# Kernel optimization log

Measured on AMD Instinct MI355X. Metric: run time of the kernel, lower is better.

The kernel has to match this reference:

```python
import jax, jax.numpy as jnp
import numpy as np

B, S, R = 8, 4096, 512
E, K, ATOMS, XAR, TOPK = 64, 256, 16, 3, 2
TEMP = 1.0


def setup_inputs() -> dict:
    key = jax.random.key(0)
    k0, k1, k2, k3, k4 = jax.random.split(key, 5)
    x_latent = jax.random.normal(k0, (B, S, R), jnp.float32)
    router_w = jax.random.normal(k1, (E, R), jnp.float32) * (1.0 / np.sqrt(R))
    atoms = jax.random.normal(k2, (E, ATOMS, R), jnp.float32) * 0.01
    combo_weights = jax.random.uniform(k3, (E, K, XAR), jnp.float32) * 0.5 + 0.25
    combo_logits = jax.random.normal(k4, (E, K, XAR, ATOMS), jnp.float32) * 0.01
    return {"x_latent": x_latent, "router_w": router_w, "atoms": atoms,
            "combo_weights": combo_weights, "combo_logits": combo_logits}


def _expert_centroids(atoms, combo_weights, combo_logits):
    # Hard codeword path (vectorized over experts):
    # sign atoms -> pick argmax atom per (k, xor slot) -> weight -> sum -> sign -> mean over k
    binary = jnp.sign(atoms)                                   # [E, A, R]
    # softmax(logits/t) then argmax == argmax(logits) (monotone)
    idx = jnp.argmax(combo_logits, axis=-1)                    # [E, K, XAR]
    sel = binary[jnp.arange(E)[:, None, None], idx]            # [E, K, XAR, R]
    codewords = jnp.sign((sel * combo_weights[..., None]).sum(axis=2))  # [E, K, R]
    return codewords.mean(axis=1)                              # [E, R]


def reference(x_latent, router_w, atoms, combo_weights, combo_logits):
    t = max(TEMP, 0.1)
    router_logits = jnp.einsum('bsr,er->bse', x_latent, router_w)   # [B, S, E]
    probs_t = jax.nn.softmax(router_logits / t, axis=-1)
    gates, expert_ids = jax.lax.top_k(probs_t, TOPK)                # [B, S, 2]
    gates = gates / gates.sum(axis=-1, keepdims=True)

    centroids = _expert_centroids(atoms, combo_weights, combo_logits)  # [E, R]

    # aux load-balancing loss (uses untempered softmax)
    router_prob = jax.nn.softmax(router_logits, axis=-1)
    aux_loss = E * jnp.sum(router_prob.mean(axis=(0, 1)) *
                           (router_prob > 0).astype(x_latent.dtype).mean(axis=(0, 1)))

    # dense per-expert gate = sum over topk slots of gate * (id == e), then combine with centroids
    dense_gates = (jax.nn.one_hot(expert_ids, E, dtype=gates.dtype) *
                   gates[..., None]).sum(axis=-2)                    # [B, S, E]
    combined = jnp.einsum('bse,er->bsr', dense_gates, centroids)     # [B, S, R]
    return combined, aux_loss
```

## Files before the change

kernel.cpp:

```cpp
#include <hip/hip_runtime.h>
#include <math.h>

#define TOKENS 32768
#define RDIM 512
#define NEXP 64
#define NK 256
#define LDQ 136
#define PSTR 67
#define TAU 4.0e-3f

typedef unsigned short u16;
typedef float f32x4 __attribute__((ext_vector_type(4)));
typedef short s16x8 __attribute__((ext_vector_type(8)));

#define MFMA_B16(a, b, c) __builtin_amdgcn_mfma_f32_16x16x32_bf16(a, b, c, 0, 0, 0)

__device__ __forceinline__ void split_pack(float4 v, unsigned& h01, unsigned& h23,
                                           unsigned& l01, unsigned& l23) {
    unsigned u0 = __float_as_uint(v.x), u1 = __float_as_uint(v.y);
    unsigned u2 = __float_as_uint(v.z), u3 = __float_as_uint(v.w);
    float r0 = v.x - __uint_as_float(u0 & 0xFFFF0000u);
    float r1 = v.y - __uint_as_float(u1 & 0xFFFF0000u);
    float r2 = v.z - __uint_as_float(u2 & 0xFFFF0000u);
    float r3 = v.w - __uint_as_float(u3 & 0xFFFF0000u);
    h01 = (u0 >> 16) | (u1 & 0xFFFF0000u);
    h23 = (u2 >> 16) | (u3 & 0xFFFF0000u);
    l01 = (__float_as_uint(r0) >> 16) | (__float_as_uint(r1) & 0xFFFF0000u);
    l23 = (__float_as_uint(r2) >> 16) | (__float_as_uint(r3) & 0xFFFF0000u);
}

__device__ __forceinline__ void split8(float4 a, float4 b, s16x8& hi, s16x8& lo) {
    union U { unsigned u[4]; s16x8 v; };
    U H, L;
    split_pack(a, H.u[0], H.u[1], L.u[0], L.u[1]);
    split_pack(b, H.u[2], H.u[3], L.u[2], L.u[3]);
    hi = H.v; lo = L.v;
}

__device__ __forceinline__ void centroid_body(
    int e, int half, int tid,
    const float* __restrict__ atoms, const float* __restrict__ cw,
    const float* __restrict__ cl, float* __restrict__ cent, unsigned* pack)
{
    {
        const int k = tid;
        unsigned u = 0;
        float w3[3];
        #pragma unroll
        for (int xx = 0; xx < 3; ++xx) {
            const float* cp = cl + ((((size_t)e * NK + k) * 3 + xx) << 4);
            float v[16];
            *(float4*)(v + 0)  = *(const float4*)(cp + 0);
            *(float4*)(v + 4)  = *(const float4*)(cp + 4);
            *(float4*)(v + 8)  = *(const float4*)(cp + 8);
            *(float4*)(v + 12) = *(const float4*)(cp + 12);
            float best = v[0]; int bi = 0;
            #pragma unroll
            for (int a = 1; a < 16; ++a) {
                if (v[a] > best) { best = v[a]; bi = a; }
            }
            u |= (unsigned)bi << (4 * xx);
            w3[xx] = cw[((size_t)e * NK + k) * 3 + xx];
        }
        unsigned lut = 0;
        #pragma unroll
        for (int c = 0; c < 8; ++c) {
            float val = ((c & 1) ? -w3[0] : w3[0])
                      + ((c & 2) ? -w3[1] : w3[1])
                      + ((c & 4) ? -w3[2] : w3[2]);
            lut |= (val < 0.f ? 1u : 0u) << c;
        }
        pack[k] = u | (lut << 16);
    }

    const int r = half * 256 + tid;
    unsigned B0 = 0;
    #pragma unroll
    for (int a = 0; a < 16; ++a)
        B0 |= (atoms[((size_t)e * 16 + a) * RDIM + r] < 0.f ? 1u : 0u) << a;
    __syncthreads();

    int n0 = 0;
    #pragma unroll 2
    for (int k = 0; k < NK; k += 8) {
        unsigned pk8[8];
        #pragma unroll
        for (int j = 0; j < 8; ++j) pk8[j] = pack[k + j];
        #pragma unroll
        for (int j = 0; j < 8; ++j) {
            unsigned u  = pk8[j];
            unsigned i0 = u & 15u, i1 = (u >> 4) & 15u, i2 = (u >> 8) & 15u;
            unsigned c0 = ((B0 >> i0) & 1u) | (((B0 >> i1) & 1u) << 1) | (((B0 >> i2) & 1u) << 2);
            n0 += (u >> (16 + c0)) & 1u;
        }
    }
    cent[(size_t)e * RDIM + r] = 1.f - (float)n0 * (1.f / 128.f);
}

__global__ __launch_bounds__(256) void centroid_pack_kernel(
    const float* __restrict__ atoms,
    const float* __restrict__ cw,
    const float* __restrict__ cl,
    const float* __restrict__ w,
    float* __restrict__ cent,
    u16* __restrict__ pk_hi,
    u16* __restrict__ pk_lo,
    float* __restrict__ aux_sum,
    unsigned* __restrict__ aux_cnt)
{
    __shared__ unsigned pack[NK];
    const int tid = threadIdx.x;
    if (blockIdx.x == 0 && tid < 64) { aux_sum[tid] = 0.f; aux_cnt[tid] = 0u; }

    if (blockIdx.x < 128) {
        centroid_body(blockIdx.x >> 1, blockIdx.x & 1, tid, atoms, cw, cl, cent, pack);
    } else {
        const int gid = (blockIdx.x - 128) * 256 + tid;
        const int row = gid >> 7;
        const int k0  = (gid & 127) * 4;
        const int g   = k0 >> 5, kg = (k0 >> 3) & 3, j = k0 & 7;
        const int idx = ((g * 4 + kg) * 64 + row) * 8 + j;
        float4 wv = *(const float4*)(w + (size_t)row * RDIM + k0);
        unsigned h01, h23, l01, l23;
        split_pack(wv, h01, h23, l01, l23);
        *(uint2*)&pk_hi[idx] = make_uint2(h01, h23);
        *(uint2*)&pk_lo[idx] = make_uint2(l01, l23);
    }
}

__global__ __launch_bounds__(256, 4) void moe_fast3(
    const float* __restrict__ x,
    const u16* __restrict__ pk_hi,
    const u16* __restrict__ pk_lo,
    const float* __restrict__ w,
    const float* __restrict__ cent,
    float* __restrict__ out,
    float* __restrict__ aux_sum,
    unsigned* __restrict__ aux_cnt)
{
    __shared__ float P[32 * PSTR];
    __shared__ float candv[32 * 25];
    __shared__ int   candi[32 * 25];
    __shared__ float qsum[32 * 9];
    __shared__ float gateL[32 * 4];
    __shared__ float s_aux[64];
    __shared__ unsigned s_cnt[64];

    const int tid  = threadIdx.x;
    const int lane = tid & 63;
    const int wv   = tid >> 6;
    const int tokG = wv >> 1;
    const int expG = wv & 1;
    const int l15  = lane & 15;
    const int kq   = lane >> 4;
    const int kgrp = kq << 3;
    const int tok0 = blockIdx.x * 32;

    if (tid < 64) { s_aux[tid] = 0.f; s_cnt[tid] = 0u; }

    f32x4 acc[2];
    acc[0] = (f32x4){0.f, 0.f, 0.f, 0.f};
    acc[1] = (f32x4){0.f, 0.f, 0.f, 0.f};

    const float* xlane = x + (size_t)(tok0 + tokG * 16 + l15) * RDIM + kgrp;
    const int fb0 = kq * 512 + (expG * 32 + l15) * 8;
    const int fb1 = fb0 + 128;

    float4 preA[4], preB[4];
    #pragma unroll
    for (int i = 0; i < 4; ++i) {
        preA[i] = *(const float4*)(xlane + i * 32);
        preB[i] = *(const float4*)(xlane + i * 32 + 4);
    }
    s16x8 pbh[2][2], pbl[2][2];
    #pragma unroll
    for (int p = 0; p < 2; ++p) {
        pbh[p][0] = *(const s16x8*)(pk_hi + p * 2048 + fb0);
        pbh[p][1] = *(const s16x8*)(pk_hi + p * 2048 + fb1);
        pbl[p][0] = *(const s16x8*)(pk_lo + p * 2048 + fb0);
        pbl[p][1] = *(const s16x8*)(pk_lo + p * 2048 + fb1);
    }

    #pragma unroll
    for (int g = 0; g < 16; ++g) {
        s16x8 ah, al;
        split8(preA[g & 3], preB[g & 3], ah, al);
        if (g + 4 < 16) {
            const float* nx = xlane + (g + 4) * 32;
            preA[g & 3] = *(const float4*)(nx);
            preB[g & 3] = *(const float4*)(nx + 4);
        }
        s16x8 bh0 = pbh[g & 1][0], bl0 = pbl[g & 1][0];
        s16x8 bh1 = pbh[g & 1][1], bl1 = pbl[g & 1][1];
        if (g + 2 < 16) {
            const int o = (g + 2) * 2048;
            pbh[g & 1][0] = *(const s16x8*)(pk_hi + o + fb0);
            pbh[g & 1][1] = *(const s16x8*)(pk_hi + o + fb1);
            pbl[g & 1][0] = *(const s16x8*)(pk_lo + o + fb0);
            pbl[g & 1][1] = *(const s16x8*)(pk_lo + o + fb1);
        }
        acc[0] = MFMA_B16(ah, bh0, acc[0]);
        acc[0] = MFMA_B16(ah, bl0, acc[0]);
        acc[0] = MFMA_B16(al, bh0, acc[0]);
        acc[1] = MFMA_B16(ah, bh1, acc[1]);
        acc[1] = MFMA_B16(ah, bl1, acc[1]);
        acc[1] = MFMA_B16(al, bh1, acc[1]);
    }

    #pragma unroll
    for (int nt = 0; nt < 2; ++nt)
        #pragma unroll
        for (int i = 0; i < 4; ++i)
            P[(tokG * 16 + kq * 4 + i) * PSTR + expG * 32 + nt * 16 + l15] = acc[nt][i];
    __syncthreads();

    const int tt = tid & 31;
    const int ss = tid >> 5;
    float v[8];
    #pragma unroll
    for (int j = 0; j < 8; ++j) v[j] = P[tt * PSTR + ss * 8 + j];

    float m1 = -INFINITY, m2 = -INFINITY, m3 = -INFINITY;
    int   i1 = NEXP, i2 = NEXP, i3 = NEXP;
    #pragma unroll
    for (int j = 0; j < 8; ++j) {
        float val = v[j]; int e = ss * 8 + j;
        if (val > m1)      { m3 = m2; i3 = i2; m2 = m1; i2 = i1; m1 = val; i1 = e; }
        else if (val > m2) { m3 = m2; i3 = i2; m2 = val; i2 = e; }
        else if (val > m3) { m3 = val; i3 = e; }
    }
    candv[tt * 25 + ss * 3 + 0] = m1; candi[tt * 25 + ss * 3 + 0] = i1;
    candv[tt * 25 + ss * 3 + 1] = m2; candi[tt * 25 + ss * 3 + 1] = i2;
    candv[tt * 25 + ss * 3 + 2] = m3; candi[tt * 25 + ss * 3 + 2] = i3;
    __syncthreads();

    m1 = m2 = m3 = -INFINITY; i1 = i2 = i3 = NEXP;
    #pragma unroll
    for (int q = 0; q < 24; ++q) {
        float val = candv[tt * 25 + q]; int e = candi[tt * 25 + q];
        if (val > m1)      { m3 = m2; i3 = i2; m2 = m1; i2 = i1; m1 = val; i1 = e; }
        else if (val > m2) { m3 = m2; i3 = i2; m2 = val; i2 = e; }
        else if (val > m3) { m3 = val; i3 = e; }
    }

    float ex[8]; float ps = 0.f;
    #pragma unroll
    for (int j = 0; j < 8; ++j) { ex[j] = __expf(v[j] - m1); ps += ex[j]; }
    qsum[tt * 9 + ss] = ps;

    if (wv == 0) {
        if (lane < 32) {
            const float ed  = __expf(m2 - m1);
            const float inv = 1.f / (1.f + ed);
            gateL[tt * 4 + 0] = inv;
            gateL[tt * 4 + 1] = ed * inv;
            ((int*)gateL)[tt * 4 + 2] = i1;
            ((int*)gateL)[tt * 4 + 3] = i2;
        }
        unsigned long long bmask = __ballot(lane < 32 && (m2 - m3 < TAU));
        while (bmask) {
            const int f = __ffsll(bmask) - 1;
            bmask &= bmask - 1;
            int id3[3];
            id3[0] = __shfl(i1, f); id3[1] = __shfl(i2, f); id3[2] = __shfl(i3, f);
            const float* xrow = x + (size_t)(tok0 + f) * RDIM + lane * 8;
            float4 a0 = *(const float4*)(xrow);
            float4 a1 = *(const float4*)(xrow + 4);
            float d[3];
            #pragma unroll
            for (int jj = 0; jj < 3; ++jj) {
                const float* wrow = w + (size_t)id3[jj] * RDIM + lane * 8;
                float4 b0 = *(const float4*)(wrow);
                float4 b1 = *(const float4*)(wrow + 4);
                float p = a0.x * b0.x;
                p = fmaf(a0.y, b0.y, p); p = fmaf(a0.z, b0.z, p); p = fmaf(a0.w, b0.w, p);
                p = fmaf(a1.x, b1.x, p); p = fmaf(a1.y, b1.y, p);
                p = fmaf(a1.z, b1.z, p); p = fmaf(a1.w, b1.w, p);
                #pragma unroll
                for (int off = 32; off; off >>= 1) p += __shfl_xor(p, off);
                d[jj] = p;
            }
            int b = 0;
            if (d[1] > d[0] || (d[1] == d[0] && id3[1] < id3[0])) b = 1;
            if (d[2] > d[b] || (d[2] == d[b] && id3[2] < id3[b])) b = 2;
            int sec;
            if (b == 0)      sec = (d[1] > d[2] || (d[1] == d[2] && id3[1] < id3[2])) ? 1 : 2;
            else if (b == 1) sec = (d[0] > d[2] || (d[0] == d[2] && id3[0] < id3[2])) ? 0 : 2;
            else             sec = (d[0] > d[1] || (d[0] == d[1] && id3[0] < id3[1])) ? 0 : 1;
            if (lane == f) {
                const float ed  = __expf(d[sec] - d[b]);
                const float inv = 1.f / (1.f + ed);
                gateL[f * 4 + 0] = inv;
                gateL[f * 4 + 1] = ed * inv;
                ((int*)gateL)[f * 4 + 2] = id3[b];
                ((int*)gateL)[f * 4 + 3] = id3[sec];
            }
        }
    }
    __syncthreads();

    float Z = 0.f;
    #pragma unroll
    for (int k = 0; k < 8; ++k) Z += qsum[tt * 9 + k];
    const float invZ = 1.f / Z;
    #pragma unroll
    for (int j = 0; j < 8; ++j) P[tt * PSTR + ss * 8 + j] = ex[j] * invZ;
    __syncthreads();

    {
        const int e = tid & 63, tq = tid >> 6;
        float s = 0.f; unsigned cn = 0u;
        #pragma unroll
        for (int t = 0; t < 8; ++t) {
            float pv = P[(tq * 8 + t) * PSTR + e];
            s += pv; cn += (pv > 0.f) ? 1u : 0u;
        }
        atomicAdd(&s_aux[e], s);
        atomicAdd(&s_cnt[e], cn);
    }
    __syncthreads();
    if (tid < 64) {
        atomicAdd(aux_sum + tid, s_aux[tid]);
        atomicAdd(aux_cnt + tid, s_cnt[tid]);
    }

    {
        const int e = lane;
        #pragma unroll
        for (int s2 = 0; s2 < 8; ++s2) {
            const int t2 = wv * 8 + s2;
            float4 g4 = *(float4*)&gateL[t2 * 4];
            const float g1 = g4.x, g2 = g4.y;
            const int e1 = __float_as_int(g4.z), e2 = __float_as_int(g4.w);
            const float4* c1 = (const float4*)(cent + (size_t)e1 * RDIM);
            const float4* c2 = (const float4*)(cent + (size_t)e2 * RDIM);
            float4* op = (float4*)(out + (size_t)(tok0 + t2) * RDIM);
            float4 A0 = c1[e],      Bb0 = c2[e];
            float4 A1 = c1[e + 64], Bb1 = c2[e + 64];
            float4 o0, o1;
            o0.x = fmaf(g1, A0.x, g2 * Bb0.x); o0.y = fmaf(g1, A0.y, g2 * Bb0.y);
            o0.z = fmaf(g1, A0.z, g2 * Bb0.z); o0.w = fmaf(g1, A0.w, g2 * Bb0.w);
            o1.x = fmaf(g1, A1.x, g2 * Bb1.x); o1.y = fmaf(g1, A1.y, g2 * Bb1.y);
            o1.z = fmaf(g1, A1.z, g2 * Bb1.z); o1.w = fmaf(g1, A1.w, g2 * Bb1.w);
            op[e]      = o0;
            op[e + 64] = o1;
        }
    }
}

__global__ __launch_bounds__(256) void centroid_kernel(
    const float* __restrict__ atoms,
    const float* __restrict__ cw,
    const float* __restrict__ cl,
    float* __restrict__ cent,
    float* __restrict__ aux_sum,
    unsigned* __restrict__ aux_cnt)
{
    __shared__ unsigned pack[NK];
    const int tid = threadIdx.x;
    if (blockIdx.x == 0 && tid < 64) { aux_sum[tid] = 0.f; aux_cnt[tid] = 0u; }
    centroid_body(blockIdx.x >> 1, blockIdx.x & 1, tid, atoms, cw, cl, cent, pack);
}

__global__ __launch_bounds__(256, 4) void moe_main(
    const float* __restrict__ x,
    const float* __restrict__ w,
    const float* __restrict__ cent,
    float* __restrict__ out,
    float* __restrict__ aux_sum,
    unsigned* __restrict__ aux_cnt)
{
    __shared__ u16 wlds[2 * 64 * LDQ];
    u16* whi = wlds;
    u16* wlo = wlds + 64 * LDQ;
    float* P     = (float*)wlds;
    float* candv = P + 64 * PSTR;
    int*   candi = (int*)(candv + 64 * 13);
    float* qsum  = (float*)(candi + 64 * 13);
    float* gateL = qsum + 64 * 5;
    __shared__ float s_aux[64];
    __shared__ unsigned s_cnt[64];

    const int tid  = threadIdx.x;
    const int lane = tid & 63;
    const int wave = tid >> 6;
    const int l15  = lane & 15;
    const int kgrp = (lane >> 4) << 3;
    const int tok0 = blockIdx.x * 64;

    if (tid < 64) { s_aux[tid] = 0.f; s_cnt[tid] = 0u; }

    f32x4 acc[4];
    #pragma unroll
    for (int nt = 0; nt < 4; ++nt) acc[nt] = (f32x4){0.f, 0.f, 0.f, 0.f};

    const float* xlane = x + (size_t)(tok0 + wave * 16 + l15) * RDIM + kgrp;
    const int wrow = tid >> 2;
    const int wseg = tid & 3;
    const float* wg = w + (size_t)wrow * RDIM + wseg * 32;
    const int woff = wrow * LDQ + wseg * 32;

    float4 preA[4], preB[4];
    #pragma unroll
    for (int i = 0; i < 4; ++i) {
        preA[i] = *(const float4*)(xlane + i * 32);
        preB[i] = *(const float4*)(xlane + i * 32 + 4);
    }

    #pragma unroll
    for (int q = 0; q < 4; ++q) {
        if (q) __syncthreads();
        {
            const float* wq = wg + q * 128;
            uint2 h2[2], l2[2];
            #pragma unroll
            for (int j = 0; j < 8; ++j) {
                float4 wvv = *(const float4*)(wq + j * 4);
                split_pack(wvv, h2[j & 1].x, h2[j & 1].y, l2[j & 1].x, l2[j & 1].y);
                if (j & 1) {
                    *(uint4*)&whi[woff + (j - 1) * 4] =
                        make_uint4(h2[0].x, h2[0].y, h2[1].x, h2[1].y);
                    *(uint4*)&wlo[woff + (j - 1) * 4] =
                        make_uint4(l2[0].x, l2[0].y, l2[1].x, l2[1].y);
                }
            }
        }
        __syncthreads();

        #pragma unroll
        for (int kb = 0; kb < 4; ++kb) {
            const int g = q * 4 + kb;
            s16x8 ah, al;
            split8(preA[g & 3], preB[g & 3], ah, al);
            if (g + 4 < 16) {
                const float* nx = xlane + (g + 4) * 32;
                preA[g & 3] = *(const float4*)(nx);
                preB[g & 3] = *(const float4*)(nx + 4);
            }
            const int kl = kb * 32 + kgrp;
            #pragma unroll
            for (int nt = 0; nt < 4; ++nt) {
                const int brow = nt * 16 + l15;
                s16x8 bh = *(const s16x8*)&whi[brow * LDQ + kl];
                s16x8 bl = *(const s16x8*)&wlo[brow * LDQ + kl];
                acc[nt] = MFMA_B16(ah, bh, acc[nt]);
                acc[nt] = MFMA_B16(ah, bl, acc[nt]);
                acc[nt] = MFMA_B16(al, bh, acc[nt]);
            }
        }
    }

    __syncthreads();
    #pragma unroll
    for (int nt = 0; nt < 4; ++nt)
        #pragma unroll
        for (int i = 0; i < 4; ++i)
            P[(wave * 16 + ((lane >> 4) << 2) + i) * PSTR + nt * 16 + l15] = acc[nt][i];
    __syncthreads();

    const int tt = tid & 63;
    const int ss = tid >> 6;
    float v[16];
    #pragma unroll
    for (int j = 0; j < 16; ++j) v[j] = P[tt * PSTR + ss * 16 + j];

    float m1 = -INFINITY, m2 = -INFINITY, m3 = -INFINITY;
    int   i1 = NEXP, i2 = NEXP, i3 = NEXP;
    #pragma unroll
    for (int j = 0; j < 16; ++j) {
        float val = v[j]; int e = ss * 16 + j;
        if (val > m1)      { m3 = m2; i3 = i2; m2 = m1; i2 = i1; m1 = val; i1 = e; }
        else if (val > m2) { m3 = m2; i3 = i2; m2 = val; i2 = e; }
        else if (val > m3) { m3 = val; i3 = e; }
    }
    candv[tt * 13 + ss * 3 + 0] = m1; candi[tt * 13 + ss * 3 + 0] = i1;
    candv[tt * 13 + ss * 3 + 1] = m2; candi[tt * 13 + ss * 3 + 1] = i2;
    candv[tt * 13 + ss * 3 + 2] = m3; candi[tt * 13 + ss * 3 + 2] = i3;
    __syncthreads();

    m1 = m2 = m3 = -INFINITY; i1 = i2 = i3 = NEXP;
    #pragma unroll
    for (int q = 0; q < 12; ++q) {
        float val = candv[tt * 13 + q]; int e = candi[tt * 13 + q];
        if (val > m1)      { m3 = m2; i3 = i2; m2 = m1; i2 = i1; m1 = val; i1 = e; }
        else if (val > m2) { m3 = m2; i3 = i2; m2 = val; i2 = e; }
        else if (val > m3) { m3 = val; i3 = e; }
    }

    float ex[16]; float ps = 0.f;
    #pragma unroll
    for (int j = 0; j < 16; ++j) { ex[j] = __expf(v[j] - m1); ps += ex[j]; }
    qsum[tt * 5 + ss] = ps;

    if (ss == 0) {
        {
            const float ed  = __expf(m2 - m1);
            const float inv = 1.f / (1.f + ed);
            gateL[tt * 4 + 0] = inv;
            gateL[tt * 4 + 1] = ed * inv;
            ((int*)gateL)[tt * 4 + 2] = i1;
            ((int*)gateL)[tt * 4 + 3] = i2;
        }
        unsigned long long bmask = __ballot(m2 - m3 < TAU);
        while (bmask) {
            const int f = __ffsll(bmask) - 1;
            bmask &= bmask - 1;
            int id3[3];
            id3[0] = __shfl(i1, f); id3[1] = __shfl(i2, f); id3[2] = __shfl(i3, f);
            const float* xrow = x + (size_t)(tok0 + f) * RDIM + lane * 8;
            float4 a0 = *(const float4*)(xrow);
            float4 a1 = *(const float4*)(xrow + 4);
            float d[3];
            #pragma unroll
            for (int jj = 0; jj < 3; ++jj) {
                const float* wrow2 = w + (size_t)id3[jj] * RDIM + lane * 8;
                float4 b0 = *(const float4*)(wrow2);
                float4 b1 = *(const float4*)(wrow2 + 4);
                float p = a0.x * b0.x;
                p = fmaf(a0.y, b0.y, p); p = fmaf(a0.z, b0.z, p); p = fmaf(a0.w, b0.w, p);
                p = fmaf(a1.x, b1.x, p); p = fmaf(a1.y, b1.y, p);
                p = fmaf(a1.z, b1.z, p); p = fmaf(a1.w, b1.w, p);
                #pragma unroll
                for (int off = 32; off; off >>= 1) p += __shfl_xor(p, off);
                d[jj] = p;
            }
            int b = 0;
            if (d[1] > d[0] || (d[1] == d[0] && id3[1] < id3[0])) b = 1;
            if (d[2] > d[b] || (d[2] == d[b] && id3[2] < id3[b])) b = 2;
            int sec;
            if (b == 0)      sec = (d[1] > d[2] || (d[1] == d[2] && id3[1] < id3[2])) ? 1 : 2;
            else if (b == 1) sec = (d[0] > d[2] || (d[0] == d[2] && id3[0] < id3[2])) ? 0 : 2;
            else             sec = (d[0] > d[1] || (d[0] == d[1] && id3[0] < id3[1])) ? 0 : 1;
            if (lane == f) {
                const float ed  = __expf(d[sec] - d[b]);
                const float inv = 1.f / (1.f + ed);
                gateL[f * 4 + 0] = inv;
                gateL[f * 4 + 1] = ed * inv;
                ((int*)gateL)[f * 4 + 2] = id3[b];
                ((int*)gateL)[f * 4 + 3] = id3[sec];
            }
        }
    }
    __syncthreads();

    float Z = 0.f;
    #pragma unroll
    for (int k = 0; k < 4; ++k) Z += qsum[tt * 5 + k];
    const float invZ = 1.f / Z;
    #pragma unroll
    for (int j = 0; j < 16; ++j) P[tt * PSTR + ss * 16 + j] = ex[j] * invZ;
    __syncthreads();

    {
        const int e = tid & 63, tq = tid >> 6;
        float s = 0.f; unsigned cn = 0u;
        #pragma unroll
        for (int t = 0; t < 16; ++t) {
            float pv = P[(tq * 16 + t) * PSTR + e];
            s += pv; cn += (pv > 0.f) ? 1u : 0u;
        }
        atomicAdd(&s_aux[e], s);
        atomicAdd(&s_cnt[e], cn);
    }
    __syncthreads();
    if (tid < 64) {
        atomicAdd(aux_sum + tid, s_aux[tid]);
        atomicAdd(aux_cnt + tid, s_cnt[tid]);
    }

    {
        const int e = lane;
        #pragma unroll
        for (int s2 = 0; s2 < 16; ++s2) {
            const int t2 = wave * 16 + s2;
            float4 g4 = *(float4*)&gateL[t2 * 4];
            const float g1 = g4.x, g2 = g4.y;
            const int e1 = __float_as_int(g4.z), e2 = __float_as_int(g4.w);
            const float4* c1 = (const float4*)(cent + (size_t)e1 * RDIM);
            const float4* c2 = (const float4*)(cent + (size_t)e2 * RDIM);
            float4* op = (float4*)(out + (size_t)(tok0 + t2) * RDIM);
            float4 A0 = c1[e],      Bb0 = c2[e];
            float4 A1 = c1[e + 64], Bb1 = c2[e + 64];
            float4 o0, o1;
            o0.x = fmaf(g1, A0.x, g2 * Bb0.x); o0.y = fmaf(g1, A0.y, g2 * Bb0.y);
            o0.z = fmaf(g1, A0.z, g2 * Bb0.z); o0.w = fmaf(g1, A0.w, g2 * Bb0.w);
            o1.x = fmaf(g1, A1.x, g2 * Bb1.x); o1.y = fmaf(g1, A1.y, g2 * Bb1.y);
            o1.z = fmaf(g1, A1.z, g2 * Bb1.z); o1.w = fmaf(g1, A1.w, g2 * Bb1.w);
            op[e]      = o0;
            op[e + 64] = o1;
        }
    }
}

__global__ __launch_bounds__(64) void aux_kernel(
    const float* __restrict__ sums,
    const unsigned* __restrict__ cnts,
    float* __restrict__ out_aux)
{
    const int e = threadIdx.x;
    float v = (sums[e] * (1.f / (float)TOKENS)) * ((float)cnts[e] * (1.f / (float)TOKENS));
    #pragma unroll
    for (int off = 32; off; off >>= 1) v += __shfl_xor(v, off);
    if (e == 0) out_aux[0] = (float)NEXP * v;
}

extern "C" void kernel_launch(void* const* d_in, const int* in_sizes, int n_in,
                              void* d_out, int out_size, void* d_ws, size_t ws_size,
                              hipStream_t stream) {
    const float* x     = (const float*)d_in[0];
    const float* rw    = (const float*)d_in[1];
    const float* atoms = (const float*)d_in[2];
    const float* cwts  = (const float*)d_in[3];
    const float* clog  = (const float*)d_in[4];
    float* out = (float*)d_out;
    float* out_aux = out + (size_t)TOKENS * RDIM;

    float*    aux_sum = (float*)d_ws;
    unsigned* aux_cnt = (unsigned*)((char*)d_ws + 256);
    float*    cent    = (float*)((char*)d_ws + 512);
    u16*      pk_hi   = (u16*)((char*)d_ws + 512 + 131072);
    u16*      pk_lo   = (u16*)((char*)d_ws + 512 + 131072 + 65536);
    const bool fast = ws_size >= (size_t)(512 + 131072 + 2 * 65536);

    if (fast) {
        centroid_pack_kernel<<<160, 256, 0, stream>>>(atoms, cwts, clog, rw, cent,
                                                      pk_hi, pk_lo, aux_sum, aux_cnt);
        moe_fast3<<<1024, 256, 0, stream>>>(x, pk_hi, pk_lo, rw, cent, out, aux_sum, aux_cnt);
    } else {
        centroid_kernel<<<128, 256, 0, stream>>>(atoms, cwts, clog, cent, aux_sum, aux_cnt);
        moe_main<<<512, 256, 0, stream>>>(x, rw, cent, out, aux_sum, aux_cnt);
    }
    aux_kernel<<<1, 64, 0, stream>>>(aux_sum, aux_cnt, out_aux);
}
```

Measured before the change: 170.4 us.

## Stage packed router weights in LDS and double tokens per block

The router GEMM now copies the bf16 hi/lo packed router weights into a 64 KB shared buffer with direct global-to-LDS loads, in two K halves. All waves then read the B fragments from LDS instead of each wave fetching them from global memory or L2. Blocks grow to 512 threads covering 64 tokens, so each staged weight tile is reused by four token groups. The softmax/top-k scratch arrays alias the same LDS buffer. The cost is extra barriers around each stage and much higher LDS use per block, which caps occupancy at only a couple of blocks per CU.

```diff
diff --git a/kernel.cpp b/kernel.cpp
--- a/kernel.cpp
+++ b/kernel.cpp
@@ -14,6 +14,12 @@
 typedef short s16x8 __attribute__((ext_vector_type(8)));
 
 #define MFMA_B16(a, b, c) __builtin_amdgcn_mfma_f32_16x16x32_bf16(a, b, c, 0, 0, 0)
+
+__device__ __forceinline__ void gload_lds16(const u16* g, u16* l) {
+    __builtin_amdgcn_global_load_lds(
+        (const __attribute__((address_space(1))) void*)g,
+        (__attribute__((address_space(3))) void*)l, 16, 0, 0);
+}
 
 __device__ __forceinline__ void split_pack(float4 v, unsigned& h01, unsigned& h23,
                                            unsigned& l01, unsigned& l23) {
@@ -128,7 +134,7 @@
     }
 }
 
-__global__ __launch_bounds__(256, 4) void moe_fast3(
+__global__ __launch_bounds__(512, 4) void moe_fast4(
     const float* __restrict__ x,
     const u16* __restrict__ pk_hi,
     const u16* __restrict__ pk_lo,
@@ -138,11 +144,14 @@
     float* __restrict__ aux_sum,
     unsigned* __restrict__ aux_cnt)
 {
-    __shared__ float P[32 * PSTR];
-    __shared__ float candv[32 * 25];
-    __shared__ int   candi[32 * 25];
-    __shared__ float qsum[32 * 9];
-    __shared__ float gateL[32 * 4];
+    __shared__ __align__(16) u16 wlds[32768];
+    u16* whi = wlds;
+    u16* wlo = wlds + 16384;
+    float* P     = (float*)wlds;
+    float* candv = P + 64 * PSTR;
+    int*   candi = (int*)(candv + 64 * 25);
+    float* qsum  = (float*)(candi + 64 * 25);
+    float* gateL = qsum + 64 * 9;
     __shared__ float s_aux[64];
     __shared__ unsigned s_cnt[64];
 
@@ -154,7 +163,7 @@
     const int l15  = lane & 15;
     const int kq   = lane >> 4;
     const int kgrp = kq << 3;
-    const int tok0 = blockIdx.x * 32;
+    const int tok0 = blockIdx.x * 64;
 
     if (tid < 64) { s_aux[tid] = 0.f; s_cnt[tid] = 0u; }
 
@@ -163,50 +172,53 @@
     acc[1] = (f32x4){0.f, 0.f, 0.f, 0.f};
 
     const float* xlane = x + (size_t)(tok0 + tokG * 16 + l15) * RDIM + kgrp;
-    const int fb0 = kq * 512 + (expG * 32 + l15) * 8;
-    const int fb1 = fb0 + 128;
-
-    float4 preA[4], preB[4];
-    #pragma unroll
-    for (int i = 0; i < 4; ++i) {
-        preA[i] = *(const float4*)(xlane + i * 32);
-        preB[i] = *(const float4*)(xlane + i * 32 + 4);
-    }
-    s16x8 pbh[2][2], pbl[2][2];
-    #pragma unroll
-    for (int p = 0; p < 2; ++p) {
-        pbh[p][0] = *(const s16x8*)(pk_hi + p * 2048 + fb0);
-        pbh[p][1] = *(const s16x8*)(pk_hi + p * 2048 + fb1);
-        pbl[p][0] = *(const s16x8*)(pk_lo + p * 2048 + fb0);
-        pbl[p][1] = *(const s16x8*)(pk_lo + p * 2048 + fb1);
-    }
-
-    #pragma unroll
-    for (int g = 0; g < 16; ++g) {
-        s16x8 ah, al;
-        split8(preA[g & 3], preB[g & 3], ah, al);
-        if (g + 4 < 16) {
-            const float* nx = xlane + (g + 4) * 32;
-            preA[g & 3] = *(const float4*)(nx);
-            preB[g & 3] = *(const float4*)(nx + 4);
-        }
-        s16x8 bh0 = pbh[g & 1][0], bl0 = pbl[g & 1][0];
-        s16x8 bh1 = pbh[g & 1][1], bl1 = pbl[g & 1][1];
-        if (g + 2 < 16) {
-            const int o = (g + 2) * 2048;
-            pbh[g & 1][0] = *(const s16x8*)(pk_hi + o + fb0);
-            pbh[g & 1][1] = *(const s16x8*)(pk_hi + o + fb1);
-            pbl[g & 1][0] = *(const s16x8*)(pk_lo + o + fb0);
-            pbl[g & 1][1] = *(const s16x8*)(pk_lo + o + fb1);
-        }
-        acc[0] = MFMA_B16(ah, bh0, acc[0]);
-        acc[0] = MFMA_B16(ah, bl0, acc[0]);
-        acc[0] = MFMA_B16(al, bh0, acc[0]);
-        acc[1] = MFMA_B16(ah, bh1, acc[1]);
-        acc[1] = MFMA_B16(ah, bl1, acc[1]);
-        acc[1] = MFMA_B16(al, bh1, acc[1]);
-    }
-
+    const int wbase = wv * 2048;
+    const int fb = (expG * 32 + l15) * 8;
+
+    #pragma unroll
+    for (int h = 0; h < 2; ++h) {
+        const float* xb = xlane + h * 256;
+        float4 p0a = *(const float4*)(xb);      float4 p0b = *(const float4*)(xb + 4);
+        float4 p1a = *(const float4*)(xb + 32); float4 p1b = *(const float4*)(xb + 36);
+        float4 p2a = *(const float4*)(xb + 64); float4 p2b = *(const float4*)(xb + 68);
+
+        __syncthreads();
+        {
+            const u16* sh = pk_hi + h * 16384 + wbase + lane * 8;
+            const u16* sl = pk_lo + h * 16384 + wbase + lane * 8;
+            #pragma unroll
+            for (int i = 0; i < 4; ++i) {
+                gload_lds16(sh + i * 512, whi + wbase + i * 512);
+                gload_lds16(sl + i * 512, wlo + wbase + i * 512);
+            }
+        }
+        __syncthreads();
+
+        #pragma unroll
+        for (int kb = 0; kb < 8; ++kb) {
+            s16x8 ah, al;
+            split8(p0a, p0b, ah, al);
+            p0a = p1a; p0b = p1b; p1a = p2a; p1b = p2b;
+            if (kb < 5) {
+                const float* nx = xb + (kb + 3) * 32;
+                p2a = *(const float4*)(nx);
+                p2b = *(const float4*)(nx + 4);
+            }
+            const int fq = (kb * 4 + kq) * 512 + fb;
+            s16x8 bh0 = *(const s16x8*)&whi[fq];
+            s16x8 bl0 = *(const s16x8*)&wlo[fq];
+            s16x8 bh1 = *(const s16x8*)&whi[fq + 128];
+            s16x8 bl1 = *(const s16x8*)&wlo[fq + 128];
+            acc[0] = MFMA_B16(ah, bh0, acc[0]);
+            acc[0] = MFMA_B16(ah, bl0, acc[0]);
+            acc[0] = MFMA_B16(al, bh0, acc[0]);
+            acc[1] = MFMA_B16(ah, bh1, acc[1]);
+            acc[1] = MFMA_B16(ah, bl1, acc[1]);
+            acc[1] = MFMA_B16(al, bh1, acc[1]);
+        }
+    }
+
+    __syncthreads();
     #pragma unroll
     for (int nt = 0; nt < 2; ++nt)
         #pragma unroll
@@ -214,8 +226,8 @@
             P[(tokG * 16 + kq * 4 + i) * PSTR + expG * 32 + nt * 16 + l15] = acc[nt][i];
     __syncthreads();
 
-    const int tt = tid & 31;
-    const int ss = tid >> 5;
+    const int tt = tid & 63;
+    const int ss = tid >> 6;
     float v[8];
     #pragma unroll
     for (int j = 0; j < 8; ++j) v[j] = P[tt * PSTR + ss * 8 + j];
@@ -248,8 +260,8 @@
     for (int j = 0; j < 8; ++j) { ex[j] = __expf(v[j] - m1); ps += ex[j]; }
     qsum[tt * 9 + ss] = ps;
 
-    if (wv == 0) {
-        if (lane < 32) {
+    if (ss == 0) {
+        {
             const float ed  = __expf(m2 - m1);
             const float inv = 1.f / (1.f + ed);
             gateL[tt * 4 + 0] = inv;
@@ -257,7 +269,7 @@
             ((int*)gateL)[tt * 4 + 2] = i1;
             ((int*)gateL)[tt * 4 + 3] = i2;
         }
-        unsigned long long bmask = __ballot(lane < 32 && (m2 - m3 < TAU));
+        unsigned long long bmask = __ballot(m2 - m3 < TAU);
         while (bmask) {
             const int f = __ffsll(bmask) - 1;
             bmask &= bmask - 1;
@@ -625,7 +637,7 @@
     if (fast) {
         centroid_pack_kernel<<<160, 256, 0, stream>>>(atoms, cwts, clog, rw, cent,
                                                       pk_hi, pk_lo, aux_sum, aux_cnt);
-        moe_fast3<<<1024, 256, 0, stream>>>(x, pk_hi, pk_lo, rw, cent, out, aux_sum, aux_cnt);
+        moe_fast4<<<512, 512, 0, stream>>>(x, pk_hi, pk_lo, rw, cent, out, aux_sum, aux_cnt);
     } else {
         centroid_kernel<<<128, 256, 0, stream>>>(atoms, cwts, clog, cent, aux_sum, aux_cnt);
         moe_main<<<512, 256, 0, stream>>>(x, rw, cent, out, aux_sum, aux_cnt);
```

Measured after the change: 154.1 us (median of 2 runs). -9.6%, faster.
